# Kernel tuning notes

Measured on AMD Instinct MI355X. Metric: run time of the kernel, lower is better.

## Reference

```python
import jax, jax.numpy as jnp
import numpy as np

L, B, S, D, H, DH, I, M = 4, 8, 1024, 256, 8, 32, 1024, 4
EPS = 1e-12


def setup_inputs() -> dict:
    key = jax.random.key(0)
    ks = jax.random.split(key, 12)

    def nrm(k, shape, scale=0.02):
        return jax.random.normal(k, shape, jnp.float32) * scale

    x = jax.random.randint(ks[0], (B, S), 0, M + 1)  # POVM outcome tokens + start token

    # sinusoidal positional encoding buffer [S, D]
    pos = np.arange(S, dtype=np.float32)[:, None]
    div = np.exp(np.arange(0, D, 2, dtype=np.float32) * (-np.log(10000.0) / D))
    pe_np = np.zeros((S, D), np.float32)
    pe_np[:, 0::2] = np.sin(pos * div)
    pe_np[:, 1::2] = np.cos(pos * div)

    return {
        "x": x,
        "emb_w": nrm(ks[1], (M + 1, D)),
        "pe": jnp.asarray(pe_np),
        "q_w": nrm(ks[2], (L, D, D)), "q_b": jnp.zeros((L, D)),
        "k_w": nrm(ks[3], (L, D, D)), "k_b": jnp.zeros((L, D)),
        "v_w": nrm(ks[4], (L, D, D)), "v_b": jnp.zeros((L, D)),
        "o_w": nrm(ks[5], (L, D, D)), "o_b": jnp.zeros((L, D)),
        "ln1_g": jnp.ones((L, D)), "ln1_b": jnp.zeros((L, D)),
        "f1_w": nrm(ks[6], (L, I, D)), "f1_b": jnp.zeros((L, I)),
        "f2_w": nrm(ks[7], (L, D, I)), "f2_b": jnp.zeros((L, D)),
        "ln2_g": jnp.ones((L, D)), "ln2_b": jnp.zeros((L, D)),
        "out_w": nrm(ks[8], (M, D)), "out_b": jnp.zeros((M,)),
    }


def _ln(x, g, b):
    m = jnp.mean(x, -1, keepdims=True)
    v = jnp.mean((x - m) ** 2, -1, keepdims=True)
    return g * (x - m) * jax.lax.rsqrt(v + EPS) + b


def reference(x, emb_w, pe, q_w, q_b, k_w, k_b, v_w, v_b, o_w, o_b,
              ln1_g, ln1_b, f1_w, f1_b, f2_w, f2_b, ln2_g, ln2_b,
              out_w, out_b):
    h = emb_w[x] + pe[None, :S, :]                       # [B,S,D]
    mask = jnp.triu(jnp.full((S, S), -1e9, jnp.float32), 1)  # causal look-ahead
    scale = 1.0 / jnp.sqrt(jnp.float32(DH))

    for l in range(L):
        # multi-head self-attention (torch Linear: x @ W.T + b)
        q = (h @ q_w[l].T + q_b[l]).reshape(B, S, H, DH)
        k = (h @ k_w[l].T + k_b[l]).reshape(B, S, H, DH)
        v = (h @ v_w[l].T + v_b[l]).reshape(B, S, H, DH)
        scores = jnp.einsum('bqhd,bkhd->bhqk', q, k) * scale + mask
        probs = jax.nn.softmax(scores, axis=-1)
        ctx = jnp.einsum('bhqk,bkhd->bqhd', probs, v).reshape(B, S, D)
        attn_out = _ln(ctx @ o_w[l].T + o_b[l] + h, ln1_g[l], ln1_b[l])
        # feed-forward sublayer
        ff = jax.nn.gelu(attn_out @ f1_w[l].T + f1_b[l], approximate=False)
        h = _ln(ff @ f2_w[l].T + f2_b[l] + attn_out, ln2_g[l], ln2_b[l])

    logits = h @ out_w.T + out_b                          # [B,S,M]
    return logits
```

## Files before the change

kernel.cpp:

```cpp
#include <hip/hip_runtime.h>
#include <cstdint>
#include <cstddef>

#define SS 1024
#define DD 256

typedef unsigned short u16;
typedef __bf16 bf16x8 __attribute__((ext_vector_type(8)));
typedef float f32x4 __attribute__((ext_vector_type(4)));
typedef unsigned short us4 __attribute__((ext_vector_type(4)));

typedef __attribute__((address_space(3))) void lds_void_t;
typedef __attribute__((address_space(1))) const void gvoid_t;

__device__ __forceinline__ u16 f2bf(float f) {
  unsigned u = __builtin_bit_cast(unsigned, f);
  u += 0x7fffu + ((u >> 16) & 1u);
  return (u16)(u >> 16);
}
__device__ __forceinline__ u16 f2bf_fast(float f) {
  unsigned u = __builtin_bit_cast(unsigned, f) + 0x8000u;
  return (u16)(u >> 16);
}
__device__ __forceinline__ float bf2f(u16 h) {
  return __builtin_bit_cast(float, ((unsigned)h) << 16);
}
__device__ __forceinline__ void gld_lds16(const void* g, void* l) {
  __builtin_amdgcn_global_load_lds((gvoid_t*)g, (lds_void_t*)l, 16, 0, 0);
}
template <int CTRL>
__device__ __forceinline__ float dppf(float x) {
  int i = __builtin_bit_cast(int, x);
  int r = __builtin_amdgcn_update_dpp(i, i, CTRL, 0xf, 0xf, false);
  return __builtin_bit_cast(float, r);
}
__device__ __forceinline__ float row_sum16(float v) {
  v += dppf<0x121>(v);
  v += dppf<0x122>(v);
  v += dppf<0x124>(v);
  v += dppf<0x128>(v);
  return v;
}
__device__ __forceinline__ float gelu_f(float x) {
  float x2 = x * x;
  float y = x * (0.7978845608028654f + 0.0356774081363f * x2);
  float e = exp2f(fminf(-2.8853900817779268f * y, 88.f));
  float th = (1.f - e) * __builtin_amdgcn_rcpf(1.f + e);
  return 0.5f * x * (1.f + th);
}

struct CvtArgs {
  const float* src[9];
  void* dst[9];
  int n4[9];
  int bf[9];
};

__global__ __launch_bounds__(256) void cvt_kernel(CvtArgs a) {
  int g = blockIdx.y;
  int i = blockIdx.x * 256 + threadIdx.x;
  if (i >= a.n4[g]) return;
  float4 v = ((const float4*)a.src[g])[i];
  if (a.bf[g]) {
    us4 o; o.x = f2bf(v.x); o.y = f2bf(v.y); o.z = f2bf(v.z); o.w = f2bf(v.w);
    ((us4*)a.dst[g])[i] = o;
  } else {
    ((float4*)a.dst[g])[i] = v;
  }
}

__global__ __launch_bounds__(256)
void embed_kernel(const int* __restrict__ x, const float* __restrict__ emb,
                  const float* __restrict__ pe, u16* __restrict__ h) {
  int wave = threadIdx.x >> 6, lane = threadIdx.x & 63;
  int row = blockIdx.x * 4 + wave;
  int s = row & (SS - 1);
  int tok = x[row];
  float4 e = *(const float4*)(emb + (size_t)tok * DD + lane * 4);
  float4 p = *(const float4*)(pe + (size_t)s * DD + lane * 4);
  us4 o; o.x = f2bf(e.x + p.x); o.y = f2bf(e.y + p.y);
  o.z = f2bf(e.z + p.z); o.w = f2bf(e.w + p.w);
  *(us4*)(h + (size_t)row * DD + lane * 4) = o;
}

enum { EPI_BIAS = 0, EPI_GELU = 1 };

#define Q_SCALE (0.17677669529663689f * 1.4426950408889634f)

template <int BM, int BN, int EPI, bool QKV>
__global__ __launch_bounds__(256)
void gemm_kernel(const u16* __restrict__ A, const u16* __restrict__ W,
                 const float* __restrict__ bias, void* __restrict__ outp,
                 u16* __restrict__ vt_out, int M, int N, int K) {
  const int n0 = blockIdx.x * BN;
  const int m0 = blockIdx.y * BM;
  const int tid = threadIdx.x;
  const int lane = tid & 63;
  const int l15 = lane & 15;
  const int quad = lane >> 4;
  const int wave = tid >> 6;
  const int wrow = wave >> 1, wcol = wave & 1;
  constexpr int WN = BN / 2;
  constexpr int NT = WN / 16;

  const u16* Wp = W;
  const float* biasp = bias;
  u16* out16 = (u16*)outp;
  int zid = 0;
  if constexpr (QKV) {
    zid = blockIdx.z;
    Wp += (size_t)zid * 262144;
    biasp += (size_t)zid * 1024;
    out16 += (size_t)zid * 2097152;
  }

  __shared__ __align__(16) u16 lds[(BM + BN) * 64];
  char* ldsA = (char*)lds;
  char* ldsB = (char*)lds + BM * 128;

  const f32x4 fzero = {0.f, 0.f, 0.f, 0.f};
  f32x4 acc[4][NT];
#pragma unroll
  for (int i = 0; i < 4; ++i)
#pragma unroll
    for (int j = 0; j < NT; ++j) acc[i][j] = fzero;

  for (int kb = 0; kb < K; kb += 64) {
    __syncthreads();
#pragma unroll
    for (int r = 0; r < BM * 8 / 256; ++r) {
      int c = r * 256 + tid;
      int row = c >> 3, slot = c & 7;
      int gc = slot ^ (row & 7);
      gld_lds16((const char*)(A + (size_t)(m0 + row) * K + kb) + gc * 16,
                ldsA + c * 16);
    }
#pragma unroll
    for (int r = 0; r < BN * 8 / 256; ++r) {
      int c = r * 256 + tid;
      int row = c >> 3, slot = c & 7;
      int gc = slot ^ (row & 7);
      gld_lds16((const char*)(Wp + (size_t)(n0 + row) * K + kb) + gc * 16,
                ldsB + c * 16);
    }
    __syncthreads();
#pragma unroll
    for (int kk = 0; kk < 2; ++kk) {
      bf16x8 af[4], bfr[NT];
#pragma unroll
      for (int i = 0; i < 4; ++i) {
        int row = wrow * 64 + i * 16 + l15;
        int slot = (kk * 4 + quad) ^ (row & 7);
        af[i] = *(const bf16x8*)(ldsA + row * 128 + slot * 16);
      }
#pragma unroll
      for (int j = 0; j < NT; ++j) {
        int row = wcol * WN + j * 16 + l15;
        int slot = (kk * 4 + quad) ^ (row & 7);
        bfr[j] = *(const bf16x8*)(ldsB + row * 128 + slot * 16);
      }
#pragma unroll
      for (int i = 0; i < 4; ++i)
#pragma unroll
        for (int j = 0; j < NT; ++j)
          acc[i][j] = __builtin_amdgcn_mfma_f32_16x16x32_bf16(af[i], bfr[j],
                                                              acc[i][j], 0, 0, 0);
    }
  }
  if (QKV && zid == 2) {
#pragma unroll
    for (int i = 0; i < 4; ++i) {
      int rbase = m0 + wrow * 64 + i * 16 + quad * 4;
      int bidx = rbase >> 10, s0 = rbase & 1023;
#pragma unroll
      for (int j = 0; j < NT; ++j) {
        int col = n0 + wcol * WN + j * 16 + l15;
        float bj = biasp[col];
        us4 o;
        o.x = f2bf(acc[i][j][0] + bj);
        o.y = f2bf(acc[i][j][1] + bj);
        o.z = f2bf(acc[i][j][2] + bj);
        o.w = f2bf(acc[i][j][3] + bj);
        *(us4*)(vt_out + ((size_t)(bidx * 8 + (col >> 5)) * 32 + (col & 31)) * SS + s0) = o;
      }
    }
    return;
  }
  const float oscale = (QKV && zid == 0) ? Q_SCALE : 1.0f;
#pragma unroll
  for (int i = 0; i < 4; ++i) {
    int rbase = m0 + wrow * 64 + i * 16 + quad * 4;
#pragma unroll
    for (int j = 0; j < NT; ++j) {
      int col = n0 + wcol * WN + j * 16 + l15;
      float bj = biasp[col];
#pragma unroll
      for (int r = 0; r < 4; ++r) {
        size_t idx = (size_t)(rbase + r) * N + col;
        float v = acc[i][j][r] + bj;
        if constexpr (EPI == EPI_GELU) {
          out16[idx] = f2bf(gelu_f(v));
        } else {
          out16[idx] = f2bf(v * oscale);
        }
      }
    }
  }
}

template <int K, bool LAST>
__global__ __launch_bounds__(256)
void gemmln_kernel(const u16* __restrict__ A, const u16* __restrict__ W,
                   const float* __restrict__ bias, const u16* __restrict__ res,
                   const float* __restrict__ g, const float* __restrict__ bta,
                   u16* __restrict__ out, const float* __restrict__ ow,
                   const float* __restrict__ obias, float* __restrict__ outp) {
  const int m0 = blockIdx.x * 16;
  const int tid = threadIdx.x;
  const int l15 = tid & 15;
  const int quad = (tid & 63) >> 4;
  const int wave = tid >> 6;

  __shared__ __align__(16) u16 lds[(16 + 256) * 64];
  char* ldsA = (char*)lds;
  char* ldsB = (char*)lds + 16 * 128;

  const f32x4 fzero = {0.f, 0.f, 0.f, 0.f};
  f32x4 acc[4];
#pragma unroll
  for (int j = 0; j < 4; ++j) acc[j] = fzero;

  for (int kb = 0; kb < K; kb += 64) {
    __syncthreads();
    if (tid < 128) {
      int c = tid;
      int row = c >> 3, slot = c & 7;
      int gc = slot ^ (row & 7);
      gld_lds16((const char*)(A + (size_t)(m0 + row) * K + kb) + gc * 16,
                ldsA + c * 16);
    }
#pragma unroll
    for (int r = 0; r < 8; ++r) {
      int c = r * 256 + tid;
      int row = c >> 3, slot = c & 7;
      int gc = slot ^ (row & 7);
      gld_lds16((const char*)(W + (size_t)row * K + kb) + gc * 16,
                ldsB + c * 16);
    }
    __syncthreads();
#pragma unroll
    for (int kk = 0; kk < 2; ++kk) {
      bf16x8 af, bfr[4];
      {
        int row = l15;
        int slot = (kk * 4 + quad) ^ (row & 7);
        af = *(const bf16x8*)(ldsA + row * 128 + slot * 16);
      }
#pragma unroll
      for (int j = 0; j < 4; ++j) {
        int row = wave * 64 + j * 16 + l15;
        int slot = (kk * 4 + quad) ^ (row & 7);
        bfr[j] = *(const bf16x8*)(ldsB + row * 128 + slot * 16);
      }
#pragma unroll
      for (int j = 0; j < 4; ++j)
        acc[j] = __builtin_amdgcn_mfma_f32_16x16x32_bf16(af, bfr[j], acc[j], 0, 0, 0);
    }
  }
  float sm[4], sq[4];
#pragma unroll
  for (int r = 0; r < 4; ++r) { sm[r] = 0.f; sq[r] = 0.f; }
#pragma unroll
  for (int j = 0; j < 4; ++j) {
    int col = wave * 64 + j * 16 + l15;
    float bj = bias[col];
#pragma unroll
    for (int r = 0; r < 4; ++r) {
      int grow = m0 + quad * 4 + r;
      float v = acc[j][r] + bj + bf2f(res[(size_t)grow * DD + col]);
      acc[j][r] = v;
      sm[r] += v;
      sq[r] += v * v;
    }
  }
#pragma unroll
  for (int r = 0; r < 4; ++r) {
    sm[r] = row_sum16(sm[r]);
    sq[r] = row_sum16(sq[r]);
  }
  __syncthreads();
  float* sred = (float*)lds;
  if (l15 == 0) {
#pragma unroll
    for (int r = 0; r < 4; ++r) {
      int ri = quad * 4 + r;
      sred[wave * 32 + ri] = sm[r];
      sred[wave * 32 + 16 + ri] = sq[r];
    }
  }
  __syncthreads();
  float mean[4], rstd[4];
#pragma unroll
  for (int r = 0; r < 4; ++r) {
    int ri = quad * 4 + r;
    float S = sred[ri] + sred[32 + ri] + sred[64 + ri] + sred[96 + ri];
    float S2 = sred[16 + ri] + sred[48 + ri] + sred[80 + ri] + sred[112 + ri];
    float mu = S * (1.f / 256.f);
    mean[r] = mu;
    rstd[r] = rsqrtf(S2 * (1.f / 256.f) - mu * mu + 1e-12f);
  }
  if constexpr (!LAST) {
#pragma unroll
    for (int j = 0; j < 4; ++j) {
      int col = wave * 64 + j * 16 + l15;
      float gj = g[col], bj = bta[col];
#pragma unroll
      for (int r = 0; r < 4; ++r) {
        int grow = m0 + quad * 4 + r;
        float v = (acc[j][r] - mean[r]) * rstd[r] * gj + bj;
        out[(size_t)grow * DD + col] = f2bf(v);
      }
    }
  } else {
    float lg[4][4];
#pragma unroll
    for (int r = 0; r < 4; ++r)
#pragma unroll
      for (int m = 0; m < 4; ++m) lg[r][m] = 0.f;
#pragma unroll
    for (int j = 0; j < 4; ++j) {
      int col = wave * 64 + j * 16 + l15;
      float gj = g[col], bj = bta[col];
      float wm[4];
#pragma unroll
      for (int m = 0; m < 4; ++m) wm[m] = ow[m * 256 + col];
#pragma unroll
      for (int r = 0; r < 4; ++r) {
        float v = (acc[j][r] - mean[r]) * rstd[r] * gj + bj;
#pragma unroll
        for (int m = 0; m < 4; ++m) lg[r][m] += v * wm[m];
      }
    }
#pragma unroll
    for (int r = 0; r < 4; ++r)
#pragma unroll
      for (int m = 0; m < 4; ++m) lg[r][m] = row_sum16(lg[r][m]);
    __syncthreads();
    float* sredh = (float*)lds;
    if (l15 == 0) {
#pragma unroll
      for (int r = 0; r < 4; ++r)
#pragma unroll
        for (int m = 0; m < 4; ++m)
          sredh[wave * 64 + (quad * 4 + r) * 4 + m] = lg[r][m];
    }
    __syncthreads();
    if (tid < 64) {
      int rr = tid >> 2, m = tid & 3;
      float s = sredh[rr * 4 + m] + sredh[64 + rr * 4 + m] +
                sredh[128 + rr * 4 + m] + sredh[192 + rr * 4 + m] + obias[m];
      outp[(size_t)(m0 + rr) * 4 + m] = s;
    }
  }
}

__global__ __launch_bounds__(256)
void attn_kernel(const u16* __restrict__ Q, const u16* __restrict__ Km,
                 const u16* __restrict__ Vt, u16* __restrict__ ctx) {
  const int tid = threadIdx.x;
  const int l15 = tid & 15;
  const int quad = (tid & 63) >> 4;
  const int wave = tid >> 6;
  const int y = blockIdx.y;
  const int qt = 15 - (((int)blockIdx.x + ((y >> 4) << 2)) & 15);
  const int q0 = qt * 64;
  const int b = y >> 3, h = y & 7;
  const int q0w = q0 + wave * 16;

  __shared__ __align__(16) u16 sK[2][64 * 40];
  __shared__ __align__(16) u16 sV[2][32 * 72];
  __shared__ __align__(16) u16 sP[4][16 * 72];
  u16* sPw = sP[wave];

  bf16x8 qf = *(const bf16x8*)(Q + ((size_t)(b * SS + q0w + l15)) * DD + h * 32 + quad * 8);

  const int krow = tid >> 2, kch = tid & 3;
  const int vd = tid >> 3, vch = tid & 7;
  const u16* Kbase = Km + (size_t)(b * SS) * DD + h * 32;
  const u16* Vbase = Vt + ((size_t)y * 32 + vd) * SS;

  uint4 kreg = *(const uint4*)(Kbase + (size_t)krow * DD + kch * 8);
  uint4 vreg = *(const uint4*)(Vbase + vch * 8);

  f32x4 o0 = {0.f, 0.f, 0.f, 0.f}, o1 = {0.f, 0.f, 0.f, 0.f};
  const f32x4 fzero = {0.f, 0.f, 0.f, 0.f};
  float rs[4] = {0.f, 0.f, 0.f, 0.f};

  const int nt = q0 >> 6;
  for (int it = 0; it <= nt; ++it) {
    const int bsel = it & 1;
    *(uint4*)((char*)sK[bsel] + krow * 80 + kch * 16) = kreg;
    *(uint4*)((char*)sV[bsel] + vd * 144 + vch * 16) = vreg;
    if (it < nt) {
      int kb = (it + 1) * 64;
      kreg = *(const uint4*)(Kbase + (size_t)(kb + krow) * DD + kch * 8);
      vreg = *(const uint4*)(Vbase + kb + vch * 8);
    }
    __syncthreads();

    f32x4 s4[4];
#pragma unroll
    for (int t = 0; t < 4; ++t) {
      bf16x8 kf = *(const bf16x8*)((const char*)sK[bsel] + (t * 16 + l15) * 80 + quad * 16);
      s4[t] = __builtin_amdgcn_mfma_f32_16x16x32_bf16(qf, kf, fzero, 0, 0, 0);
    }
    if (it == nt) {
#pragma unroll
      for (int t = 0; t < 4; ++t) {
        int key = it * 64 + t * 16 + l15;
#pragma unroll
        for (int r = 0; r < 4; ++r) {
          int qr = q0w + quad * 4 + r;
          float p = exp2f(s4[t][r]);
          p = (key > qr) ? 0.f : p;
          s4[t][r] = p;
          rs[r] += p;
        }
      }
    } else {
#pragma unroll
      for (int t = 0; t < 4; ++t)
#pragma unroll
        for (int r = 0; r < 4; ++r) {
          float p = exp2f(s4[t][r]);
          s4[t][r] = p;
          rs[r] += p;
        }
    }
#pragma unroll
    for (int t = 0; t < 4; ++t)
#pragma unroll
      for (int r = 0; r < 4; ++r)
        sPw[(quad * 4 + r) * 72 + t * 16 + l15] = f2bf_fast(s4[t][r]);
#pragma unroll
    for (int kt = 0; kt < 2; ++kt) {
      bf16x8 pf = *(const bf16x8*)((char*)sPw + l15 * 144 + kt * 64 + quad * 16);
      bf16x8 v0 = *(const bf16x8*)((const char*)sV[bsel] + l15 * 144 + kt * 64 + quad * 16);
      bf16x8 v1 = *(const bf16x8*)((const char*)sV[bsel] + (16 + l15) * 144 + kt * 64 + quad * 16);
      o0 = __builtin_amdgcn_mfma_f32_16x16x32_bf16(pf, v0, o0, 0, 0, 0);
      o1 = __builtin_amdgcn_mfma_f32_16x16x32_bf16(pf, v1, o1, 0, 0, 0);
    }
  }
#pragma unroll
  for (int r = 0; r < 4; ++r) {
    float inv = 1.0f / row_sum16(rs[r]);
    int q = q0w + quad * 4 + r;
    size_t base = ((size_t)(b * SS + q)) * DD + h * 32;
    ctx[base + l15] = f2bf(o0[r] * inv);
    ctx[base + 16 + l15] = f2bf(o1[r] * inv);
  }
}

extern "C" void kernel_launch(void* const* d_in, const int* in_sizes, int n_in,
                              void* d_out, int out_size, void* d_ws, size_t ws_size,
                              hipStream_t stream) {
  const int* x = (const int*)d_in[0];
  const float* emb_w = (const float*)d_in[1];
  const float* pe = (const float*)d_in[2];
  const float* q_w = (const float*)d_in[3];
  const float* q_b = (const float*)d_in[4];
  const float* k_w = (const float*)d_in[5];
  const float* k_b = (const float*)d_in[6];
  const float* v_w = (const float*)d_in[7];
  const float* v_b = (const float*)d_in[8];
  const float* o_w = (const float*)d_in[9];
  const float* o_b = (const float*)d_in[10];
  const float* ln1_g = (const float*)d_in[11];
  const float* ln1_b = (const float*)d_in[12];
  const float* f1_w = (const float*)d_in[13];
  const float* f1_b = (const float*)d_in[14];
  const float* f2_w = (const float*)d_in[15];
  const float* f2_b = (const float*)d_in[16];
  const float* ln2_g = (const float*)d_in[17];
  const float* ln2_b = (const float*)d_in[18];
  const float* out_w = (const float*)d_in[19];
  const float* out_b = (const float*)d_in[20];
  float* out = (float*)d_out;

  char* w = (char*)d_ws;
  const size_t MB = 1ull << 20;
  u16* hb    = (u16*)(w + 0 * MB);
  u16* qb    = (u16*)(w + 4 * MB);
  u16* kbuf  = (u16*)(w + 8 * MB);
  u16* vtb   = (u16*)(w + 12 * MB);
  u16* ctxb  = (u16*)(w + 16 * MB);
  u16* attnb = (u16*)(w + 20 * MB);
  u16* ffb   = (u16*)(w + 24 * MB);
  u16* wqkv  = (u16*)(w + 48 * MB);
  u16* wo    = (u16*)(w + 50 * MB);
  u16* wf1   = (u16*)(w + 51 * MB);
  u16* wf2   = (u16*)(w + 53 * MB);
  float* bqkv = (float*)(w + 55 * MB);

  CvtArgs ca;
  ca.src[0] = q_w;  ca.dst[0] = wqkv;            ca.n4[0] = 65536;  ca.bf[0] = 1;
  ca.src[1] = k_w;  ca.dst[1] = wqkv + 262144;   ca.n4[1] = 65536;  ca.bf[1] = 1;
  ca.src[2] = v_w;  ca.dst[2] = wqkv + 524288;   ca.n4[2] = 65536;  ca.bf[2] = 1;
  ca.src[3] = o_w;  ca.dst[3] = wo;              ca.n4[3] = 65536;  ca.bf[3] = 1;
  ca.src[4] = f1_w; ca.dst[4] = wf1;             ca.n4[4] = 262144; ca.bf[4] = 1;
  ca.src[5] = f2_w; ca.dst[5] = wf2;             ca.n4[5] = 262144; ca.bf[5] = 1;
  ca.src[6] = q_b;  ca.dst[6] = bqkv;            ca.n4[6] = 256;    ca.bf[6] = 0;
  ca.src[7] = k_b;  ca.dst[7] = bqkv + 1024;     ca.n4[7] = 256;    ca.bf[7] = 0;
  ca.src[8] = v_b;  ca.dst[8] = bqkv + 2048;     ca.n4[8] = 256;    ca.bf[8] = 0;
  cvt_kernel<<<dim3(1024, 9), 256, 0, stream>>>(ca);

  embed_kernel<<<2048, 256, 0, stream>>>(x, emb_w, pe, hb);

  for (int l = 0; l < 4; ++l) {
    const size_t wofs = (size_t)l * 65536;
    const size_t fofs = (size_t)l * 262144;
    gemm_kernel<128, 64, EPI_BIAS, true><<<dim3(4, 64, 3), 256, 0, stream>>>(
        hb, wqkv + wofs, bqkv + l * 256, qb, vtb, 8192, 256, 256);
    attn_kernel<<<dim3(16, 64), 256, 0, stream>>>(qb, kbuf, vtb, ctxb);
    gemmln_kernel<256, false><<<512, 256, 0, stream>>>(
        ctxb, wo + wofs, o_b + l * 256, hb, ln1_g + l * 256, ln1_b + l * 256,
        attnb, nullptr, nullptr, nullptr);
    gemm_kernel<128, 128, EPI_GELU, false><<<dim3(8, 64), 256, 0, stream>>>(
        attnb, wf1 + fofs, f1_b + l * 1024, ffb, nullptr, 8192, 1024, 256);
    if (l < 3) {
      gemmln_kernel<1024, false><<<512, 256, 0, stream>>>(
          ffb, wf2 + fofs, f2_b + l * 256, attnb, ln2_g + l * 256,
          ln2_b + l * 256, hb, nullptr, nullptr, nullptr);
    } else {
      gemmln_kernel<1024, true><<<512, 256, 0, stream>>>(
          ffb, wf2 + fofs, f2_b + l * 256, attnb, ln2_g + l * 256,
          ln2_b + l * 256, hb, out_w, out_b, out);
    }
  }
}
```

Baseline: 381.3 us.

## Transpose attention MFMA layout, merge embed into convert kernel, shrink FFN1 tile

The attention kernel swaps the MFMA operands so each lane owns one query row. This lets the row sum be a single scalar reduced with two shuffles, P be written to LDS as packed 8-byte stores, and ctx be written with vector stores instead of scattered 16-bit stores. The embedding kernel is folded into the weight-convert launch as an extra grid slice, which removes one launch. The grid grows to 2048 blocks, so many convert blocks exit early. The FFN1 GEMM drops from 128x128 to 128x64 tiles, doubling the block count for more parallelism at the cost of less reuse.

```diff
diff --git a/kernel.cpp b/kernel.cpp
--- a/kernel.cpp
+++ b/kernel.cpp
@@ -18,12 +18,13 @@
   u += 0x7fffu + ((u >> 16) & 1u);
   return (u16)(u >> 16);
 }
-__device__ __forceinline__ u16 f2bf_fast(float f) {
-  unsigned u = __builtin_bit_cast(unsigned, f) + 0x8000u;
-  return (u16)(u >> 16);
-}
 __device__ __forceinline__ float bf2f(u16 h) {
   return __builtin_bit_cast(float, ((unsigned)h) << 16);
+}
+__device__ __forceinline__ unsigned pack2bf(float a, float b) {
+  unsigned ua = __builtin_bit_cast(unsigned, a) + 0x8000u;
+  unsigned ub = __builtin_bit_cast(unsigned, b) + 0x8000u;
+  return (ua >> 16) | (ub & 0xffff0000u);
 }
 __device__ __forceinline__ void gld_lds16(const void* g, void* l) {
   __builtin_amdgcn_global_load_lds((gvoid_t*)g, (lds_void_t*)l, 16, 0, 0);
@@ -56,8 +57,23 @@
   int bf[9];
 };
 
-__global__ __launch_bounds__(256) void cvt_kernel(CvtArgs a) {
+__global__ __launch_bounds__(256)
+void cvt_kernel(CvtArgs a, const int* __restrict__ x,
+                const float* __restrict__ emb, const float* __restrict__ pe,
+                u16* __restrict__ h) {
   int g = blockIdx.y;
+  if (g == 9) {
+    int wave = threadIdx.x >> 6, lane = threadIdx.x & 63;
+    int row = blockIdx.x * 4 + wave;
+    int s = row & (SS - 1);
+    int tok = x[row];
+    float4 e = *(const float4*)(emb + (size_t)tok * DD + lane * 4);
+    float4 p = *(const float4*)(pe + (size_t)s * DD + lane * 4);
+    us4 o; o.x = f2bf(e.x + p.x); o.y = f2bf(e.y + p.y);
+    o.z = f2bf(e.z + p.z); o.w = f2bf(e.w + p.w);
+    *(us4*)(h + (size_t)row * DD + lane * 4) = o;
+    return;
+  }
   int i = blockIdx.x * 256 + threadIdx.x;
   if (i >= a.n4[g]) return;
   float4 v = ((const float4*)a.src[g])[i];
@@ -67,20 +83,6 @@
   } else {
     ((float4*)a.dst[g])[i] = v;
   }
-}
-
-__global__ __launch_bounds__(256)
-void embed_kernel(const int* __restrict__ x, const float* __restrict__ emb,
-                  const float* __restrict__ pe, u16* __restrict__ h) {
-  int wave = threadIdx.x >> 6, lane = threadIdx.x & 63;
-  int row = blockIdx.x * 4 + wave;
-  int s = row & (SS - 1);
-  int tok = x[row];
-  float4 e = *(const float4*)(emb + (size_t)tok * DD + lane * 4);
-  float4 p = *(const float4*)(pe + (size_t)s * DD + lane * 4);
-  us4 o; o.x = f2bf(e.x + p.x); o.y = f2bf(e.y + p.y);
-  o.z = f2bf(e.z + p.z); o.w = f2bf(e.w + p.w);
-  *(us4*)(h + (size_t)row * DD + lane * 4) = o;
 }
 
 enum { EPI_BIAS = 0, EPI_GELU = 1 };
@@ -394,7 +396,8 @@
 
   f32x4 o0 = {0.f, 0.f, 0.f, 0.f}, o1 = {0.f, 0.f, 0.f, 0.f};
   const f32x4 fzero = {0.f, 0.f, 0.f, 0.f};
-  float rs[4] = {0.f, 0.f, 0.f, 0.f};
+  float rs = 0.f;
+  const int myq = q0w + l15;
 
   const int nt = q0 >> 6;
   for (int it = 0; it <= nt; ++it) {
@@ -412,19 +415,18 @@
 #pragma unroll
     for (int t = 0; t < 4; ++t) {
       bf16x8 kf = *(const bf16x8*)((const char*)sK[bsel] + (t * 16 + l15) * 80 + quad * 16);
-      s4[t] = __builtin_amdgcn_mfma_f32_16x16x32_bf16(qf, kf, fzero, 0, 0, 0);
+      s4[t] = __builtin_amdgcn_mfma_f32_16x16x32_bf16(kf, qf, fzero, 0, 0, 0);
     }
     if (it == nt) {
 #pragma unroll
       for (int t = 0; t < 4; ++t) {
-        int key = it * 64 + t * 16 + l15;
+        int kbase = it * 64 + t * 16 + quad * 4;
 #pragma unroll
         for (int r = 0; r < 4; ++r) {
-          int qr = q0w + quad * 4 + r;
           float p = exp2f(s4[t][r]);
-          p = (key > qr) ? 0.f : p;
+          p = (kbase + r > myq) ? 0.f : p;
           s4[t][r] = p;
-          rs[r] += p;
+          rs += p;
         }
       }
     } else {
@@ -434,31 +436,37 @@
         for (int r = 0; r < 4; ++r) {
           float p = exp2f(s4[t][r]);
           s4[t][r] = p;
-          rs[r] += p;
+          rs += p;
         }
     }
 #pragma unroll
-    for (int t = 0; t < 4; ++t)
-#pragma unroll
-      for (int r = 0; r < 4; ++r)
-        sPw[(quad * 4 + r) * 72 + t * 16 + l15] = f2bf_fast(s4[t][r]);
+    for (int t = 0; t < 4; ++t) {
+      uint2 pk;
+      pk.x = pack2bf(s4[t][0], s4[t][1]);
+      pk.y = pack2bf(s4[t][2], s4[t][3]);
+      *(uint2*)((char*)sPw + l15 * 144 + t * 32 + quad * 8) = pk;
+    }
 #pragma unroll
     for (int kt = 0; kt < 2; ++kt) {
       bf16x8 pf = *(const bf16x8*)((char*)sPw + l15 * 144 + kt * 64 + quad * 16);
       bf16x8 v0 = *(const bf16x8*)((const char*)sV[bsel] + l15 * 144 + kt * 64 + quad * 16);
       bf16x8 v1 = *(const bf16x8*)((const char*)sV[bsel] + (16 + l15) * 144 + kt * 64 + quad * 16);
-      o0 = __builtin_amdgcn_mfma_f32_16x16x32_bf16(pf, v0, o0, 0, 0, 0);
-      o1 = __builtin_amdgcn_mfma_f32_16x16x32_bf16(pf, v1, o1, 0, 0, 0);
-    }
-  }
+      o0 = __builtin_amdgcn_mfma_f32_16x16x32_bf16(v0, pf, o0, 0, 0, 0);
+      o1 = __builtin_amdgcn_mfma_f32_16x16x32_bf16(v1, pf, o1, 0, 0, 0);
+    }
+  }
+  rs += __shfl_xor(rs, 16);
+  rs += __shfl_xor(rs, 32);
+  float inv = 1.0f / rs;
+  size_t base = ((size_t)(b * SS + myq)) * DD + h * 32;
+  us4 w0, w1;
 #pragma unroll
   for (int r = 0; r < 4; ++r) {
-    float inv = 1.0f / row_sum16(rs[r]);
-    int q = q0w + quad * 4 + r;
-    size_t base = ((size_t)(b * SS + q)) * DD + h * 32;
-    ctx[base + l15] = f2bf(o0[r] * inv);
-    ctx[base + 16 + l15] = f2bf(o1[r] * inv);
-  }
+    ((u16*)&w0)[r] = f2bf(o0[r] * inv);
+    ((u16*)&w1)[r] = f2bf(o1[r] * inv);
+  }
+  *(us4*)(ctx + base + quad * 4) = w0;
+  *(us4*)(ctx + base + 16 + quad * 4) = w1;
 }
 
 extern "C" void kernel_launch(void* const* d_in, const int* in_sizes, int n_in,
@@ -512,9 +520,7 @@
   ca.src[6] = q_b;  ca.dst[6] = bqkv;            ca.n4[6] = 256;    ca.bf[6] = 0;
   ca.src[7] = k_b;  ca.dst[7] = bqkv + 1024;     ca.n4[7] = 256;    ca.bf[7] = 0;
   ca.src[8] = v_b;  ca.dst[8] = bqkv + 2048;     ca.n4[8] = 256;    ca.bf[8] = 0;
-  cvt_kernel<<<dim3(1024, 9), 256, 0, stream>>>(ca);
-
-  embed_kernel<<<2048, 256, 0, stream>>>(x, emb_w, pe, hb);
+  cvt_kernel<<<dim3(2048, 10), 256, 0, stream>>>(ca, x, emb_w, pe, hb);
 
   for (int l = 0; l < 4; ++l) {
     const size_t wofs = (size_t)l * 65536;
@@ -525,7 +531,7 @@
     gemmln_kernel<256, false><<<512, 256, 0, stream>>>(
         ctxb, wo + wofs, o_b + l * 256, hb, ln1_g + l * 256, ln1_b + l * 256,
         attnb, nullptr, nullptr, nullptr);
-    gemm_kernel<128, 128, EPI_GELU, false><<<dim3(8, 64), 256, 0, stream>>>(
+    gemm_kernel<128, 64, EPI_GELU, false><<<dim3(16, 64), 256, 0, stream>>>(
         attnb, wf1 + fofs, f1_b + l * 1024, ffb, nullptr, 8192, 1024, 256);
     if (l < 3) {
       gemmln_kernel<1024, false><<<512, 256, 0, stream>>>(
```

New measurement: 369.6 us. 1.03x faster.
